# Kernel tuning notes

Hardware: AMD Instinct MI355X
Metric: run time of the kernel (lower is better)

The kernel has to match this reference:

```python
import jax, jax.numpy as jnp
import numpy as np

L, D, H, M = 4, 256, 8, 1024  # num_blocks, emb_dim, num_heads, mlp_dim
B, N = 8, 1024
HD = H * D  # per-head dim == emb_dim in this module (hidden_dims = emb_dim*num_heads)


def setup_inputs() -> dict:
    key = jax.random.key(0)
    ks = jax.random.split(key, 6)
    s = 0.02
    return {
        "x": jax.random.normal(ks[0], (B, N, D), jnp.float32),
        "ln1_g": jnp.ones((L, D), jnp.float32),
        "ln1_b": jnp.zeros((L, D), jnp.float32),
        "qkv_w": jax.random.normal(ks[1], (L, D, 3 * HD), jnp.float32) * s,
        "qkv_b": jnp.zeros((L, 3 * HD), jnp.float32),
        "proj_w": jax.random.normal(ks[2], (L, HD, D), jnp.float32) * s,
        "proj_b": jnp.zeros((L, D), jnp.float32),
        "ln2_g": jnp.ones((L, D), jnp.float32),
        "ln2_b": jnp.zeros((L, D), jnp.float32),
        "w1": jax.random.normal(ks[3], (L, D, M), jnp.float32) * s,
        "b1": jnp.zeros((L, M), jnp.float32),
        "w2": jax.random.normal(ks[4], (L, M, D), jnp.float32) * s,
        "b2": jnp.zeros((L, D), jnp.float32),
    }


def _layernorm(x, g, b):
    m = x.mean(-1, keepdims=True)
    v = x.var(-1, keepdims=True)  # torch LayerNorm: biased variance, eps=1e-5
    return (x - m) * jax.lax.rsqrt(v + 1e-5) * g + b


def reference(x, ln1_g, ln1_b, qkv_w, qkv_b, proj_w, proj_b, ln2_g, ln2_b, w1, b1, w2, b2):
    b, n, d = x.shape
    scale = d ** 0.5  # source intends emb_dim**0.5; NOTE: applied AFTER softmax (bug preserved)
    for i in range(L):
        # --- attention residual block (pre-norm) ---
        h = _layernorm(x, ln1_g[i], ln1_b[i])
        qkv = (h @ qkv_w[i] + qkv_b[i]).reshape(b, n, H, d, 3)  # 'b n (h d qkv)'
        q = jnp.transpose(qkv[..., 0], (0, 2, 1, 3))  # [b,H,n,d]
        k = jnp.transpose(qkv[..., 1], (0, 2, 1, 3))
        v = jnp.transpose(qkv[..., 2], (0, 2, 1, 3))
        energy = jnp.einsum('bhqd,bhkd->bhqk', q, k)
        attn = jax.nn.softmax(energy, axis=-1) / scale  # post-softmax scaling as in source
        o = jnp.einsum('bhal,bhlv->bhav', attn, v)
        o = jnp.transpose(o, (0, 2, 1, 3)).reshape(b, n, H * d)
        x = x + (o @ proj_w[i] + proj_b[i])
        # --- MLP residual block (pre-norm) ---
        h = _layernorm(x, ln2_g[i], ln2_b[i])
        h = jax.nn.gelu(h @ w1[i] + b1[i], approximate=False)  # torch nn.GELU default = exact
        x = x + (h @ w2[i] + b2[i])
    return x
```

## Files before the change

### kernel.cpp

```cpp
#include <hip/hip_runtime.h>
#include <cstdint>
#include <cmath>

typedef float f32x4 __attribute__((ext_vector_type(4)));
typedef short s16x8 __attribute__((ext_vector_type(8)));

__device__ __forceinline__ unsigned short f2bf(float f) {
  union { float f; unsigned u; } v; v.f = f;
  unsigned r = v.u + 0x7FFFu + ((v.u >> 16) & 1u);
  return (unsigned short)(r >> 16);
}

__device__ __forceinline__ void async16(const void* g, void* l) {
  __builtin_amdgcn_global_load_lds(
      (const __attribute__((address_space(1))) unsigned int*)g,
      (__attribute__((address_space(3))) unsigned int*)l, 16, 0, 0);
}

#define MFMA(a,b,c) __builtin_amdgcn_mfma_f32_16x16x32_bf16((a),(b),(c),0,0,0)

#define Lb 4
#define Dm 256
#define Hh 8
#define Mm 1024
#define Bb 8
#define Nn 1024
#define ROWS (Bb*Nn)
#define QKVN (3*Hh*Dm)

__global__ __launch_bounds__(256) void ln_kernel(const float* __restrict__ x,
                                                 const float* __restrict__ g,
                                                 const float* __restrict__ b,
                                                 unsigned short* __restrict__ out) {
  int wave = threadIdx.x >> 6, lane = threadIdx.x & 63;
  int row = blockIdx.x * 4 + wave;
  const float4* xr = (const float4*)(x + (size_t)row * Dm);
  float4 v = xr[lane];
  float s = v.x + v.y + v.z + v.w;
  float s2 = v.x*v.x + v.y*v.y + v.z*v.z + v.w*v.w;
  #pragma unroll
  for (int off = 1; off < 64; off <<= 1) {
    s  += __shfl_xor(s,  off);
    s2 += __shfl_xor(s2, off);
  }
  float mean = s * (1.0f/Dm);
  float var  = s2 * (1.0f/Dm) - mean*mean;
  float inv  = rsqrtf(var + 1e-5f);
  float4 gg = ((const float4*)g)[lane];
  float4 bb = ((const float4*)b)[lane];
  ushort4 o;
  o.x = f2bf((v.x-mean)*inv*gg.x + bb.x);
  o.y = f2bf((v.y-mean)*inv*gg.y + bb.y);
  o.z = f2bf((v.z-mean)*inv*gg.z + bb.z);
  o.w = f2bf((v.w-mean)*inv*gg.w + bb.w);
  ((ushort4*)(out + (size_t)row * Dm))[lane] = o;
}

__global__ void conv_qkv(const float* __restrict__ w, const float* __restrict__ bsrc,
                         unsigned short* __restrict__ wt, float* __restrict__ bperm) {
  size_t idx = (size_t)blockIdx.x * 256 + threadIdx.x;
  int k = idx & 255;
  size_t t = idx >> 8;
  int n = (int)(t % QKVN);
  int l = (int)(t / QKVN);
  int c  = n >> 11;
  int hh = (n >> 8) & 7;
  int dd = n & 255;
  int j = hh*768 + dd*3 + c;
  wt[idx] = f2bf(w[((size_t)l*Dm + k)*QKVN + j]);
  if (k == 0) bperm[l*QKVN + n] = bsrc[l*QKVN + j];
}

__global__ void conv_t(const float* __restrict__ w, unsigned short* __restrict__ wt,
                       int Kd, int Nd) {
  size_t idx = (size_t)blockIdx.x * 256 + threadIdx.x;
  int k = (int)(idx % Kd);
  size_t t = idx / Kd;
  int n = (int)(t % Nd);
  int l = (int)(t / Nd);
  wt[idx] = f2bf(w[((size_t)l*Kd + k)*Nd + n]);
}

template<int EPI>
__global__ __launch_bounds__(256, 2) void gemm_bt(const unsigned short* __restrict__ A,
                                                  const unsigned short* __restrict__ Bt,
                                                  const float* __restrict__ bias,
                                                  const float* __restrict__ resid,
                                                  void* __restrict__ outv,
                                                  unsigned short* __restrict__ vtg,
                                                  int M, int N, int K) {
  constexpr int BM = 128, BN = 128, BK = 32;
  __shared__ __align__(16) unsigned short As[2][BM * BK];
  __shared__ __align__(16) unsigned short Bs[2][BN * BK];
  int tid = threadIdx.x;
  int lane = tid & 63, wave = tid >> 6;
  int wm = (wave >> 1) * 64, wn = (wave & 1) * 64;
  int mblk = blockIdx.y * BM, nblk = blockIdx.x * BN;
  int l15 = lane & 15, q4 = lane >> 4;

  f32x4 acc[4][4] = {};

  int arow = tid >> 2;
  int acol = (tid & 3) * 8;
  const unsigned short* Ag = A + (size_t)(mblk + arow) * K + acol;
  const unsigned short* Bg = Bt + (size_t)(nblk + arow) * K + acol;

  async16(Ag,                As[0] + tid*8);
  async16(Ag + (size_t)64*K, As[0] + 2048 + tid*8);
  async16(Bg,                Bs[0] + tid*8);
  async16(Bg + (size_t)64*K, Bs[0] + 2048 + tid*8);

  int nk = K / BK;
  for (int i = 0; i < nk; i++) {
    __syncthreads();
    if (i + 1 < nk) {
      int k0 = (i + 1) * BK;
      unsigned short* Asl = As[(i+1)&1] + tid*8;
      unsigned short* Bsl = Bs[(i+1)&1] + tid*8;
      async16(Ag + k0,                Asl);
      async16(Ag + (size_t)64*K + k0, Asl + 2048);
      async16(Bg + k0,                Bsl);
      async16(Bg + (size_t)64*K + k0, Bsl + 2048);
    }
    const unsigned short* Ac = As[i&1];
    const unsigned short* Bc = Bs[i&1];
    s16x8 af[4], bf[4];
    #pragma unroll
    for (int j = 0; j < 4; j++)
      af[j] = *(const s16x8*)(Ac + (wm + j*16 + l15) * BK + q4*8);
    #pragma unroll
    for (int j = 0; j < 4; j++)
      bf[j] = *(const s16x8*)(Bc + (wn + j*16 + l15) * BK + q4*8);
    #pragma unroll
    for (int mi = 0; mi < 4; mi++)
      #pragma unroll
      for (int ni = 0; ni < 4; ni++)
        acc[mi][ni] = MFMA(af[mi], bf[ni], acc[mi][ni]);
  }

  #pragma unroll
  for (int mi = 0; mi < 4; mi++)
    #pragma unroll
    for (int ni = 0; ni < 4; ni++) {
      int col = nblk + wn + ni*16 + l15;
      float bcol = bias[col];
      if (EPI == 3 && (nblk >> 11) == 2) {
        int hh = (col >> 8) & 7, dd = col & 255;
        int row0 = mblk + wm + mi*16 + q4*4;
        int bi = row0 >> 10, n0 = row0 & 1023;
        ushort4 pk;
        pk.x = f2bf(acc[mi][ni][0] + bcol);
        pk.y = f2bf(acc[mi][ni][1] + bcol);
        pk.z = f2bf(acc[mi][ni][2] + bcol);
        pk.w = f2bf(acc[mi][ni][3] + bcol);
        *(ushort4*)(vtg + ((size_t)(bi*8 + hh)*256 + dd)*1024 + n0) = pk;
      } else {
        #pragma unroll
        for (int r = 0; r < 4; r++) {
          int row = mblk + wm + mi*16 + q4*4 + r;
          float v = acc[mi][ni][r] + bcol;
          if (EPI == 0) {
            ((unsigned short*)outv)[(size_t)row * N + col] = f2bf(v);
          } else if (EPI == 1) {
            v = 0.5f * v * (1.0f + erff(v * 0.70710678118f));
            ((unsigned short*)outv)[(size_t)row * N + col] = f2bf(v);
          } else if (EPI == 2) {
            size_t idx = (size_t)row * N + col;
            ((float*)outv)[idx] = v + resid[idx];
          } else {
            ((unsigned short*)outv)[(size_t)row * 4096 + col] = f2bf(v);
          }
        }
      }
    }
}

__global__ __launch_bounds__(256, 2) void attn_kernel(const unsigned short* __restrict__ qk,
                                                      const unsigned short* __restrict__ vt,
                                                      unsigned short* __restrict__ obuf) {
  int bh = blockIdx.x;
  int b = bh >> 3, h = bh & 7;
  int qt = blockIdx.y;
  int tid = threadIdx.x, lane = tid & 63, wave = tid >> 6;
  int l15 = lane & 15, q4 = lane >> 4;

  __shared__ __align__(16) unsigned short Ks[2][32 * 256];
  __shared__ __align__(16) unsigned short Vs[2][256 * 32];

  const unsigned short* Qb  = qk + (size_t)(b * Nn) * 4096 + h * 256;
  const unsigned short* Kb  = Qb + 2048;
  const unsigned short* VTb = vt + (size_t)bh * 256 * 1024;

  int qbase = qt * 128 + wave * 32;

  s16x8 qf[2][8];
  #pragma unroll
  for (int s = 0; s < 2; s++) {
    const unsigned short* qp = Qb + (size_t)(qbase + s*16 + l15) * 4096 + q4*8;
    #pragma unroll
    for (int c = 0; c < 8; c++) qf[s][c] = *(const s16x8*)(qp + c*32);
  }

  f32x4 oacc[2][16] = {};
  float lrun[2] = {0.f, 0.f};

  int ke[4], kc_[4], ve_[4];
  #pragma unroll
  for (int ii = 0; ii < 4; ii++) {
    int e = tid*8 + ii*2048;
    ke[ii] = e;
    int ky = e >> 8, sc = (e >> 5) & 7;
    kc_[ii] = (sc ^ (ky & 7))*32 + (e & 31) + (ky << 12);
    ve_[ii] = (e >> 5) * 1024 + (e & 31);
  }

  #pragma unroll
  for (int ii = 0; ii < 4; ii++) {
    async16(Kb + kc_[ii],  Ks[0] + ke[ii]);
    async16(VTb + ve_[ii], Vs[0] + ke[ii]);
  }

  for (int kt = 0; kt < 32; kt++) {
    __syncthreads();
    if (kt + 1 < 32) {
      int buf = (kt + 1) & 1;
      #pragma unroll
      for (int ii = 0; ii < 4; ii++) {
        async16(Kb + (size_t)(kt+1)*32*4096 + kc_[ii], Ks[buf] + ke[ii]);
        async16(VTb + (kt+1)*32 + ve_[ii],             Vs[buf] + ke[ii]);
      }
    }
    const unsigned short* Kc = Ks[kt & 1];
    const unsigned short* Vc = Vs[kt & 1];

    f32x4 sacc[2][2] = {};
    #pragma unroll
    for (int c = 0; c < 8; c++)
      #pragma unroll
      for (int mb = 0; mb < 2; mb++) {
        s16x8 af = *(const s16x8*)(Kc + (mb*16 + l15)*256 + ((c ^ (l15 & 7))*32 + q4*8));
        sacc[0][mb] = MFMA(af, qf[0][c], sacc[0][mb]);
        sacc[1][mb] = MFMA(af, qf[1][c], sacc[1][mb]);
      }

    int pk[2][2][2];
    #pragma unroll
    for (int s = 0; s < 2; s++) {
      float v0[4], v1[4];
      float rs = 0.f;
      #pragma unroll
      for (int r = 0; r < 4; r++) {
        v0[r] = __expf(sacc[s][0][r] - 12.0f);
        v1[r] = __expf(sacc[s][1][r] - 12.0f);
        rs += v0[r] + v1[r];
      }
      rs += __shfl_xor(rs, 16);
      rs += __shfl_xor(rs, 32);
      lrun[s] += rs;
      pk[s][0][0] = (int)f2bf(v0[0]) | ((int)f2bf(v0[1]) << 16);
      pk[s][0][1] = (int)f2bf(v0[2]) | ((int)f2bf(v0[3]) << 16);
      pk[s][1][0] = (int)f2bf(v1[0]) | ((int)f2bf(v1[1]) << 16);
      pk[s][1][1] = (int)f2bf(v1[2]) | ((int)f2bf(v1[3]) << 16);
    }

    int src0 = l15 + 16 * ((q4 & 1) * 2);
    int src1 = src0 + 16;
    bool sel = (q4 < 2);
    s16x8 pa[2];
    #pragma unroll
    for (int s = 0; s < 2; s++) {
      int u00 = __shfl(pk[s][0][0], src0), u10 = __shfl(pk[s][1][0], src0);
      int u01 = __shfl(pk[s][0][1], src0), u11 = __shfl(pk[s][1][1], src0);
      int u02 = __shfl(pk[s][0][0], src1), u12 = __shfl(pk[s][1][0], src1);
      int u03 = __shfl(pk[s][0][1], src1), u13 = __shfl(pk[s][1][1], src1);
      union { int u[4]; s16x8 v; } P;
      P.u[0] = sel ? u00 : u10;
      P.u[1] = sel ? u01 : u11;
      P.u[2] = sel ? u02 : u12;
      P.u[3] = sel ? u03 : u13;
      pa[s] = P.v;
    }

    #pragma unroll
    for (int nb = 0; nb < 16; nb++) {
      s16x8 vf = *(const s16x8*)(Vc + (nb*16 + l15)*32 + q4*8);
      oacc[0][nb] = MFMA(pa[0], vf, oacc[0][nb]);
      oacc[1][nb] = MFMA(pa[1], vf, oacc[1][nb]);
    }
  }

  #pragma unroll
  for (int s = 0; s < 2; s++) {
    float lr[4];
    #pragma unroll
    for (int r = 0; r < 4; r++) lr[r] = __shfl(lrun[s], q4*4 + r);
    #pragma unroll
    for (int r = 0; r < 4; r++) {
      float sc = 1.0f / (lr[r] * 16.0f);
      int row = b * Nn + qbase + s*16 + q4*4 + r;
      unsigned short* op = obuf + (size_t)row * 2048 + h * 256;
      #pragma unroll
      for (int nb = 0; nb < 16; nb++)
        op[nb*16 + l15] = f2bf(oacc[s][nb][r] * sc);
    }
  }
}

extern "C" void kernel_launch(void* const* d_in, const int* in_sizes, int n_in,
                              void* d_out, int out_size, void* d_ws, size_t ws_size,
                              hipStream_t stream) {
  const float* x_in   = (const float*)d_in[0];
  const float* ln1_g  = (const float*)d_in[1];
  const float* ln1_b  = (const float*)d_in[2];
  const float* qkv_w  = (const float*)d_in[3];
  const float* qkv_b  = (const float*)d_in[4];
  const float* proj_w = (const float*)d_in[5];
  const float* proj_b = (const float*)d_in[6];
  const float* ln2_g  = (const float*)d_in[7];
  const float* ln2_b  = (const float*)d_in[8];
  const float* w1     = (const float*)d_in[9];
  const float* b1     = (const float*)d_in[10];
  const float* w2     = (const float*)d_in[11];
  const float* b2     = (const float*)d_in[12];

  char* ws = (char*)d_ws;
  size_t off = 0;
  float*          X    = (float*)(ws + off);          off += (size_t)ROWS*Dm*4;
  unsigned short* Hb   = (unsigned short*)(ws + off); off += (size_t)ROWS*Dm*2;
  unsigned short* QK   = (unsigned short*)(ws + off); off += (size_t)ROWS*4096*2;
  unsigned short* VT   = (unsigned short*)(ws + off); off += (size_t)64*256*1024*2;
  unsigned short* O    = (unsigned short*)(ws + off); off += (size_t)ROWS*2048*2;
  unsigned short* H1   = (unsigned short*)(ws + off); off += (size_t)ROWS*Mm*2;
  unsigned short* QKVW = (unsigned short*)(ws + off); off += (size_t)Lb*QKVN*Dm*2;
  float*          QKVB = (float*)(ws + off);          off += (size_t)Lb*QKVN*4;
  unsigned short* PRJW = (unsigned short*)(ws + off); off += (size_t)Lb*Dm*2048*2;
  unsigned short* W1T  = (unsigned short*)(ws + off); off += (size_t)Lb*Mm*Dm*2;
  unsigned short* W2T  = (unsigned short*)(ws + off); off += (size_t)Lb*Dm*Mm*2;

  hipMemcpyAsync(X, x_in, (size_t)ROWS*Dm*4, hipMemcpyDeviceToDevice, stream);

  conv_qkv<<<24576, 256, 0, stream>>>(qkv_w, qkv_b, QKVW, QKVB);
  conv_t<<<8192, 256, 0, stream>>>(proj_w, PRJW, 2048, 256);
  conv_t<<<4096, 256, 0, stream>>>(w1, W1T, 256, 1024);
  conv_t<<<4096, 256, 0, stream>>>(w2, W2T, 1024, 256);

  for (int l = 0; l < Lb; l++) {
    ln_kernel<<<ROWS/4, 256, 0, stream>>>(X, ln1_g + l*Dm, ln1_b + l*Dm, Hb);
    gemm_bt<3><<<dim3(QKVN/128, ROWS/128), 256, 0, stream>>>(
        Hb, QKVW + (size_t)l*QKVN*Dm, QKVB + (size_t)l*QKVN, nullptr, QK, VT,
        ROWS, QKVN, Dm);
    attn_kernel<<<dim3(Bb*Hh, Nn/128), 256, 0, stream>>>(QK, VT, O);
    gemm_bt<2><<<dim3(Dm/128, ROWS/128), 256, 0, stream>>>(
        O, PRJW + (size_t)l*Dm*2048, proj_b + l*Dm, X, X, nullptr, ROWS, Dm, 2048);
    ln_kernel<<<ROWS/4, 256, 0, stream>>>(X, ln2_g + l*Dm, ln2_b + l*Dm, Hb);
    gemm_bt<1><<<dim3(Mm/128, ROWS/128), 256, 0, stream>>>(
        Hb, W1T + (size_t)l*Mm*Dm, b1 + l*Mm, nullptr, H1, nullptr, ROWS, Mm, Dm);
    gemm_bt<2><<<dim3(Dm/128, ROWS/128), 256, 0, stream>>>(
        H1, W2T + (size_t)l*Dm*Mm, b2 + l*Dm, X, X, nullptr, ROWS, Dm, Mm);
  }

  hipMemcpyAsync(d_out, X, (size_t)ROWS*Dm*4, hipMemcpyDeviceToDevice, stream);
}
```

Before: 1.101 ms.

## Split-K narrow GEMMs with fused residual+LayerNorm combine, tiled weight transpose

The proj and MLP-down GEMMs (N=256) now use split-K across blockIdx.z (4-way and 2-way), writing fp32 partials. A new kernel sums the partials, adds the residual and applies the next LayerNorm in one pass, which replaces the separate residual epilogue and LN launches. The grid was only 128 blocks, and split-K is meant to give those narrow GEMMs enough blocks to fill the GPU. Other changes: the weight conversions use an LDS-tiled transpose for coalesced access, the V-transpose epilogue is staged through shared memory for 16-byte stores, and the attention grid order is swapped. The cost is extra partial-sum traffic.

Measured after the change: 1.064 ms. -3.4%, faster.

```diff
diff --git a/kernel.cpp b/kernel.cpp
--- a/kernel.cpp
+++ b/kernel.cpp
@@ -56,42 +56,101 @@
   ((ushort4*)(out + (size_t)row * Dm))[lane] = o;
 }
 
-__global__ void conv_qkv(const float* __restrict__ w, const float* __restrict__ bsrc,
-                         unsigned short* __restrict__ wt, float* __restrict__ bperm) {
-  size_t idx = (size_t)blockIdx.x * 256 + threadIdx.x;
-  int k = idx & 255;
-  size_t t = idx >> 8;
-  int n = (int)(t % QKVN);
-  int l = (int)(t / QKVN);
-  int c  = n >> 11;
-  int hh = (n >> 8) & 7;
-  int dd = n & 255;
-  int j = hh*768 + dd*3 + c;
-  wt[idx] = f2bf(w[((size_t)l*Dm + k)*QKVN + j]);
-  if (k == 0) bperm[l*QKVN + n] = bsrc[l*QKVN + j];
-}
-
-__global__ void conv_t(const float* __restrict__ w, unsigned short* __restrict__ wt,
-                       int Kd, int Nd) {
-  size_t idx = (size_t)blockIdx.x * 256 + threadIdx.x;
-  int k = (int)(idx % Kd);
-  size_t t = idx / Kd;
-  int n = (int)(t % Nd);
-  int l = (int)(t / Nd);
-  wt[idx] = f2bf(w[((size_t)l*Kd + k)*Nd + n]);
+__global__ __launch_bounds__(256) void lncomb_kernel(const float* __restrict__ xin,
+                                                     const float* __restrict__ pp, int nz,
+                                                     const float* __restrict__ g,
+                                                     const float* __restrict__ b,
+                                                     float* __restrict__ xout,
+                                                     unsigned short* __restrict__ hb) {
+  int wave = threadIdx.x >> 6, lane = threadIdx.x & 63;
+  int row = blockIdx.x * 4 + wave;
+  size_t base = (size_t)row * Dm;
+  float4 v = ((const float4*)(xin + base))[lane];
+  #pragma unroll 4
+  for (int z = 0; z < nz; z++) {
+    float4 p = ((const float4*)(pp + (size_t)z * ROWS * Dm + base))[lane];
+    v.x += p.x; v.y += p.y; v.z += p.z; v.w += p.w;
+  }
+  ((float4*)(xout + base))[lane] = v;
+  float s = v.x + v.y + v.z + v.w;
+  float s2 = v.x*v.x + v.y*v.y + v.z*v.z + v.w*v.w;
+  #pragma unroll
+  for (int off = 1; off < 64; off <<= 1) {
+    s  += __shfl_xor(s,  off);
+    s2 += __shfl_xor(s2, off);
+  }
+  float mean = s * (1.0f/Dm);
+  float var  = s2 * (1.0f/Dm) - mean*mean;
+  float inv  = rsqrtf(var + 1e-5f);
+  float4 gg = ((const float4*)g)[lane];
+  float4 bb = ((const float4*)b)[lane];
+  ushort4 o;
+  o.x = f2bf((v.x-mean)*inv*gg.x + bb.x);
+  o.y = f2bf((v.y-mean)*inv*gg.y + bb.y);
+  o.z = f2bf((v.z-mean)*inv*gg.z + bb.z);
+  o.w = f2bf((v.w-mean)*inv*gg.w + bb.w);
+  ((ushort4*)(hb + base))[lane] = o;
+}
+
+__global__ __launch_bounds__(256) void comb_out_kernel(const float* __restrict__ xin,
+                                                       const float* __restrict__ pp, int nz,
+                                                       float* __restrict__ out) {
+  int wave = threadIdx.x >> 6, lane = threadIdx.x & 63;
+  int row = blockIdx.x * 4 + wave;
+  size_t base = (size_t)row * Dm;
+  float4 v = ((const float4*)(xin + base))[lane];
+  #pragma unroll 4
+  for (int z = 0; z < nz; z++) {
+    float4 p = ((const float4*)(pp + (size_t)z * ROWS * Dm + base))[lane];
+    v.x += p.x; v.y += p.y; v.z += p.z; v.w += p.w;
+  }
+  ((float4*)(out + base))[lane] = v;
+}
+
+template<bool PERM>
+__global__ __launch_bounds__(256) void convT(const float* __restrict__ w,
+                                             unsigned short* __restrict__ wt,
+                                             int Kd, int Nd) {
+  __shared__ float tile[32][33];
+  int nt = blockIdx.x * 32, kt = blockIdx.y * 32, l = blockIdx.z;
+  int tx = threadIdx.x & 31, ty = threadIdx.x >> 5;
+  const float* src = w + ((size_t)l * Kd + kt) * Nd + nt;
+  #pragma unroll
+  for (int r = 0; r < 4; r++)
+    tile[ty + r*8][tx] = src[(size_t)(ty + r*8) * Nd + tx];
+  __syncthreads();
+  #pragma unroll
+  for (int r = 0; r < 4; r++) {
+    int nl = ty + r*8;
+    int j = nt + nl;
+    int n = j;
+    if (PERM) {
+      int hh = j / 768, rem = j - hh*768;
+      int dd = rem / 3, c = rem - dd*3;
+      n = c*2048 + hh*256 + dd;
+    }
+    wt[((size_t)l * Nd + n) * Kd + kt + tx] = f2bf(tile[tx][nl]);
+  }
+}
+
+__global__ void conv_bias(const float* __restrict__ bsrc, float* __restrict__ bperm) {
+  int i = blockIdx.x * 256 + threadIdx.x;
+  int l = i / QKVN, n = i - l*QKVN;
+  int c = n >> 11, hh = (n >> 8) & 7, dd = n & 255;
+  bperm[i] = bsrc[l*QKVN + hh*768 + dd*3 + c];
 }
 
 template<int EPI>
 __global__ __launch_bounds__(256, 2) void gemm_bt(const unsigned short* __restrict__ A,
                                                   const unsigned short* __restrict__ Bt,
                                                   const float* __restrict__ bias,
-                                                  const float* __restrict__ resid,
                                                   void* __restrict__ outv,
                                                   unsigned short* __restrict__ vtg,
-                                                  int M, int N, int K) {
+                                                  int M, int N, int Kstride, int Ksub) {
   constexpr int BM = 128, BN = 128, BK = 32;
   __shared__ __align__(16) unsigned short As[2][BM * BK];
   __shared__ __align__(16) unsigned short Bs[2][BN * BK];
+  __shared__ __align__(16) unsigned short vtile[(EPI == 3) ? 128 * 136 : 1];
   int tid = threadIdx.x;
   int lane = tid & 63, wave = tid >> 6;
   int wm = (wave >> 1) * 64, wn = (wave & 1) * 64;
@@ -102,25 +161,27 @@
 
   int arow = tid >> 2;
   int acol = (tid & 3) * 8;
-  const unsigned short* Ag = A + (size_t)(mblk + arow) * K + acol;
-  const unsigned short* Bg = Bt + (size_t)(nblk + arow) * K + acol;
-
-  async16(Ag,                As[0] + tid*8);
-  async16(Ag + (size_t)64*K, As[0] + 2048 + tid*8);
-  async16(Bg,                Bs[0] + tid*8);
-  async16(Bg + (size_t)64*K, Bs[0] + 2048 + tid*8);
-
-  int nk = K / BK;
+  const unsigned short* Ag = A + (size_t)blockIdx.z * Ksub
+                               + (size_t)(mblk + arow) * Kstride + acol;
+  const unsigned short* Bg = Bt + (size_t)blockIdx.z * Ksub
+                               + (size_t)(nblk + arow) * Kstride + acol;
+
+  async16(Ag,                      As[0] + tid*8);
+  async16(Ag + (size_t)64*Kstride, As[0] + 2048 + tid*8);
+  async16(Bg,                      Bs[0] + tid*8);
+  async16(Bg + (size_t)64*Kstride, Bs[0] + 2048 + tid*8);
+
+  int nk = Ksub / BK;
   for (int i = 0; i < nk; i++) {
     __syncthreads();
     if (i + 1 < nk) {
       int k0 = (i + 1) * BK;
       unsigned short* Asl = As[(i+1)&1] + tid*8;
       unsigned short* Bsl = Bs[(i+1)&1] + tid*8;
-      async16(Ag + k0,                Asl);
-      async16(Ag + (size_t)64*K + k0, Asl + 2048);
-      async16(Bg + k0,                Bsl);
-      async16(Bg + (size_t)64*K + k0, Bsl + 2048);
+      async16(Ag + k0,                      Asl);
+      async16(Ag + (size_t)64*Kstride + k0, Asl + 2048);
+      async16(Bg + k0,                      Bsl);
+      async16(Bg + (size_t)64*Kstride + k0, Bsl + 2048);
     }
     const unsigned short* Ac = As[i&1];
     const unsigned short* Bc = Bs[i&1];
@@ -138,49 +199,74 @@
         acc[mi][ni] = MFMA(af[mi], bf[ni], acc[mi][ni]);
   }
 
-  #pragma unroll
-  for (int mi = 0; mi < 4; mi++)
-    #pragma unroll
-    for (int ni = 0; ni < 4; ni++) {
-      int col = nblk + wn + ni*16 + l15;
-      float bcol = bias[col];
-      if (EPI == 3 && (nblk >> 11) == 2) {
-        int hh = (col >> 8) & 7, dd = col & 255;
-        int row0 = mblk + wm + mi*16 + q4*4;
-        int bi = row0 >> 10, n0 = row0 & 1023;
-        ushort4 pk;
-        pk.x = f2bf(acc[mi][ni][0] + bcol);
-        pk.y = f2bf(acc[mi][ni][1] + bcol);
-        pk.z = f2bf(acc[mi][ni][2] + bcol);
-        pk.w = f2bf(acc[mi][ni][3] + bcol);
-        *(ushort4*)(vtg + ((size_t)(bi*8 + hh)*256 + dd)*1024 + n0) = pk;
-      } else {
+  auto scalar_epi = [&]() {
+    #pragma unroll
+    for (int mi = 0; mi < 4; mi++)
+      #pragma unroll
+      for (int ni = 0; ni < 4; ni++) {
+        int col = nblk + wn + ni*16 + l15;
+        float bcol;
+        if (EPI == 4) bcol = (blockIdx.z == 0) ? bias[col] : 0.0f;
+        else          bcol = bias[col];
         #pragma unroll
         for (int r = 0; r < 4; r++) {
           int row = mblk + wm + mi*16 + q4*4 + r;
           float v = acc[mi][ni][r] + bcol;
-          if (EPI == 0) {
-            ((unsigned short*)outv)[(size_t)row * N + col] = f2bf(v);
-          } else if (EPI == 1) {
+          if (EPI == 1) {
             v = 0.5f * v * (1.0f + erff(v * 0.70710678118f));
             ((unsigned short*)outv)[(size_t)row * N + col] = f2bf(v);
-          } else if (EPI == 2) {
-            size_t idx = (size_t)row * N + col;
-            ((float*)outv)[idx] = v + resid[idx];
-          } else {
+          } else if (EPI == 3) {
             ((unsigned short*)outv)[(size_t)row * 4096 + col] = f2bf(v);
+          } else if (EPI == 4) {
+            float* out = (float*)outv + (size_t)blockIdx.z * M * N;
+            out[(size_t)row * N + col] = v;
           }
         }
       }
-    }
+  };
+
+  if constexpr (EPI == 3) {
+    if (nblk >= 4096) {
+      #pragma unroll
+      for (int mi = 0; mi < 4; mi++)
+        #pragma unroll
+        for (int ni = 0; ni < 4; ni++) {
+          int col_l = wn + ni*16 + l15;
+          float bcol = bias[nblk + col_l];
+          int seq_l = wm + mi*16 + q4*4;
+          ushort4 pk4;
+          pk4.x = f2bf(acc[mi][ni][0] + bcol);
+          pk4.y = f2bf(acc[mi][ni][1] + bcol);
+          pk4.z = f2bf(acc[mi][ni][2] + bcol);
+          pk4.w = f2bf(acc[mi][ni][3] + bcol);
+          *(ushort4*)(vtile + col_l * 136 + seq_l) = pk4;
+        }
+      __syncthreads();
+      int base = nblk - 4096;
+      int hh = base >> 8, ddb = base & 255;
+      int bi = mblk >> 10, n0 = mblk & 1023;
+      unsigned short* dst = vtg + ((size_t)(bi*8 + hh) * 256 + ddb) * 1024 + n0;
+      #pragma unroll
+      for (int p = 0; p < 8; p++) {
+        int flat = p * 2048 + tid * 8;
+        int ddl = flat >> 7, ns = flat & 127;
+        int4 v4 = *(const int4*)(vtile + ddl * 136 + ns);
+        *(int4*)(dst + (size_t)ddl * 1024 + ns) = v4;
+      }
+    } else {
+      scalar_epi();
+    }
+  } else {
+    scalar_epi();
+  }
 }
 
 __global__ __launch_bounds__(256, 2) void attn_kernel(const unsigned short* __restrict__ qk,
                                                       const unsigned short* __restrict__ vt,
                                                       unsigned short* __restrict__ obuf) {
-  int bh = blockIdx.x;
+  int qt = blockIdx.x;
+  int bh = blockIdx.y;
   int b = bh >> 3, h = bh & 7;
-  int qt = blockIdx.y;
   int tid = threadIdx.x, lane = tid & 63, wave = tid >> 6;
   int l15 = lane & 15, q4 = lane >> 4;
 
@@ -325,9 +411,9 @@
 
   char* ws = (char*)d_ws;
   size_t off = 0;
-  float*          X    = (float*)(ws + off);          off += (size_t)ROWS*Dm*4;
+  float*          X0   = (float*)(ws + off);          off += (size_t)ROWS*Dm*4;
   unsigned short* Hb   = (unsigned short*)(ws + off); off += (size_t)ROWS*Dm*2;
-  unsigned short* QK   = (unsigned short*)(ws + off); off += (size_t)ROWS*4096*2;
+  char*           QKre = ws + off;                    off += (size_t)ROWS*4096*2;
   unsigned short* VT   = (unsigned short*)(ws + off); off += (size_t)64*256*1024*2;
   unsigned short* O    = (unsigned short*)(ws + off); off += (size_t)ROWS*2048*2;
   unsigned short* H1   = (unsigned short*)(ws + off); off += (size_t)ROWS*Mm*2;
@@ -337,27 +423,40 @@
   unsigned short* W1T  = (unsigned short*)(ws + off); off += (size_t)Lb*Mm*Dm*2;
   unsigned short* W2T  = (unsigned short*)(ws + off); off += (size_t)Lb*Dm*Mm*2;
 
-  hipMemcpyAsync(X, x_in, (size_t)ROWS*Dm*4, hipMemcpyDeviceToDevice, stream);
-
-  conv_qkv<<<24576, 256, 0, stream>>>(qkv_w, qkv_b, QKVW, QKVB);
-  conv_t<<<8192, 256, 0, stream>>>(proj_w, PRJW, 2048, 256);
-  conv_t<<<4096, 256, 0, stream>>>(w1, W1T, 256, 1024);
-  conv_t<<<4096, 256, 0, stream>>>(w2, W2T, 1024, 256);
+  unsigned short* QK = (unsigned short*)QKre;
+  float*          PP = (float*)QKre;
+  float*          X1 = (float*)(QKre + (size_t)36*1024*1024);
+
+  hipMemcpyAsync(X0, x_in, (size_t)ROWS*Dm*4, hipMemcpyDeviceToDevice, stream);
+
+  convT<true><<<dim3(QKVN/32, Dm/32, Lb), 256, 0, stream>>>(qkv_w, QKVW, Dm, QKVN);
+  conv_bias<<<Lb*QKVN/256, 256, 0, stream>>>(qkv_b, QKVB);
+  convT<false><<<dim3(Dm/32, 2048/32, Lb), 256, 0, stream>>>(proj_w, PRJW, 2048, Dm);
+  convT<false><<<dim3(Mm/32, Dm/32, Lb), 256, 0, stream>>>(w1, W1T, Dm, Mm);
+  convT<false><<<dim3(Dm/32, Mm/32, Lb), 256, 0, stream>>>(w2, W2T, Mm, Dm);
 
   for (int l = 0; l < Lb; l++) {
-    ln_kernel<<<ROWS/4, 256, 0, stream>>>(X, ln1_g + l*Dm, ln1_b + l*Dm, Hb);
+    if (l == 0)
+      ln_kernel<<<ROWS/4, 256, 0, stream>>>(X0, ln1_g, ln1_b, Hb);
     gemm_bt<3><<<dim3(QKVN/128, ROWS/128), 256, 0, stream>>>(
-        Hb, QKVW + (size_t)l*QKVN*Dm, QKVB + (size_t)l*QKVN, nullptr, QK, VT,
-        ROWS, QKVN, Dm);
-    attn_kernel<<<dim3(Bb*Hh, Nn/128), 256, 0, stream>>>(QK, VT, O);
-    gemm_bt<2><<<dim3(Dm/128, ROWS/128), 256, 0, stream>>>(
-        O, PRJW + (size_t)l*Dm*2048, proj_b + l*Dm, X, X, nullptr, ROWS, Dm, 2048);
-    ln_kernel<<<ROWS/4, 256, 0, stream>>>(X, ln2_g + l*Dm, ln2_b + l*Dm, Hb);
+        Hb, QKVW + (size_t)l*QKVN*Dm, QKVB + (size_t)l*QKVN, QK, VT,
+        ROWS, QKVN, Dm, Dm);
+    attn_kernel<<<dim3(Nn/128, Bb*Hh), 256, 0, stream>>>(QK, VT, O);
+    gemm_bt<4><<<dim3(Dm/128, ROWS/128, 4), 256, 0, stream>>>(
+        O, PRJW + (size_t)l*Dm*2048, proj_b + l*Dm, PP, nullptr,
+        ROWS, Dm, 2048, 512);
+    lncomb_kernel<<<ROWS/4, 256, 0, stream>>>(X0, PP, 4, ln2_g + l*Dm, ln2_b + l*Dm,
+                                              X1, Hb);
     gemm_bt<1><<<dim3(Mm/128, ROWS/128), 256, 0, stream>>>(
-        Hb, W1T + (size_t)l*Mm*Dm, b1 + l*Mm, nullptr, H1, nullptr, ROWS, Mm, Dm);
-    gemm_bt<2><<<dim3(Dm/128, ROWS/128), 256, 0, stream>>>(
-        H1, W2T + (size_t)l*Dm*Mm, b2 + l*Dm, X, X, nullptr, ROWS, Dm, Mm);
-  }
-
-  hipMemcpyAsync(d_out, X, (size_t)ROWS*Dm*4, hipMemcpyDeviceToDevice, stream);
-}
+        Hb, W1T + (size_t)l*Mm*Dm, b1 + l*Mm, H1, nullptr, ROWS, Mm, Dm, Dm);
+    gemm_bt<4><<<dim3(Dm/128, ROWS/128, 2), 256, 0, stream>>>(
+        H1, W2T + (size_t)l*Dm*Mm, b2 + l*Dm, PP, nullptr,
+        ROWS, Dm, Mm, 512);
+    if (l < Lb - 1) {
+      lncomb_kernel<<<ROWS/4, 256, 0, stream>>>(X1, PP, 2, ln1_g + (l+1)*Dm,
+                                                ln1_b + (l+1)*Dm, X0, Hb);
+    } else {
+      comb_out_kernel<<<ROWS/4, 256, 0, stream>>>(X1, PP, 2, (float*)d_out);
+    }
+  }
+}
```
